# Optimization experiments

Hardware: AMD Instinct MI355X
Metric: run time of the kernel (lower is better)

Reference implementation:

```python
import jax, jax.numpy as jnp
import numpy as np

B = 32768      # batch
D = 512        # embedding dim
V = 100000     # vocab_length (row 0 reserved -> table has V+1 rows)
S = 100        # num_neg_samples (hard-coded in source)
DISTORTION = 0.4


def _expected_counts():
    # fixed_unigram sampler: zipf-ish counts, distorted by 0.4, 1 reserved id
    counts = 1.0 / np.arange(1, V + 1, dtype=np.float64)
    p = counts ** DISTORTION
    p = p / p.sum()
    q = np.zeros(V + 1, dtype=np.float64)
    # unique sampling expected count: E[id in sample] = 1-(1-p)^S
    q[1:] = -np.expm1(S * np.log1p(-p))
    q[0] = 1e-9  # reserved id, never sampled; avoid log(0)
    return q


def setup_inputs() -> dict:
    key = jax.random.key(0)
    k1, k2, k3, k4 = jax.random.split(key, 4)
    label = jax.random.randint(k1, (B,), 1, V + 1, dtype=jnp.int64)
    inputs = jax.random.normal(k2, (B, D), dtype=jnp.float32)
    weights = jax.random.normal(k3, (V + 1, D), dtype=jnp.float32) * 0.05
    biases = jnp.zeros((V + 1,), dtype=jnp.float32)
    sampled_ids = jax.random.choice(k4, V, (S,), replace=False).astype(jnp.int64) + 1
    q = jnp.asarray(_expected_counts(), dtype=jnp.float32)
    true_expected_count = q[label]          # [B]
    sampled_expected_count = q[sampled_ids]  # [S]
    return {
        "label": label, "inputs": inputs, "weights": weights, "biases": biases,
        "sampled_ids": sampled_ids,
        "true_expected_count": true_expected_count,
        "sampled_expected_count": sampled_expected_count,
    }


def reference(label, inputs, weights, biases, sampled_ids,
              true_expected_count, sampled_expected_count):
    # --- _compute_sampled_logits with subtract_log_q=True ---
    true_w = weights[label]                                   # [B, D] gather
    true_logits = (jnp.einsum('bd,bd->b', inputs, true_w)
                   + biases[label]
                   - jnp.log(true_expected_count))            # [B]
    samp_w = weights[sampled_ids]                             # [S, D] gather
    samp_logits = (jnp.einsum('bd,sd->bs', inputs, samp_w)
                   + biases[sampled_ids]
                   - jnp.log(sampled_expected_count))         # [B, S]
    logits = jnp.concatenate([true_logits[:, None], samp_logits], axis=1)  # [B, 1+S]
    # labels are one-hot at column 0 -> CE = logsumexp - true logit
    losses = jax.nn.logsumexp(logits, axis=1) - logits[:, 0]
    loss = jnp.mean(losses)
    return logits, loss
```

## Files before the change

kernel.cpp:

```cpp
#include <hip/hip_runtime.h>
#include <math.h>

#define B_TOT 32768
#define DIM   512
#define NS    100
#define NCOL  101
#define TB    128
#define NBLK  (B_TOT / TB)
#define WPITCH 520

typedef __attribute__((ext_vector_type(8))) short short8;
typedef __attribute__((ext_vector_type(4))) float f32x4;

static __device__ __forceinline__ short f2bf(float f) {
    unsigned u = __builtin_bit_cast(unsigned, f);
    unsigned r = (u + 0x7FFFu + ((u >> 16) & 1u)) >> 16;
    return (short)r;
}

__global__ __launch_bounds__(512)
void fused_kernel(const int* __restrict__ label,
                  const float* __restrict__ inputs,
                  const float* __restrict__ weights,
                  const float* __restrict__ biases,
                  const int* __restrict__ sids,
                  const float* __restrict__ tq,
                  const float* __restrict__ sq,
                  float* __restrict__ out,
                  float* __restrict__ lpart)
{
    __shared__ short W_lds[112 * WPITCH];
    __shared__ float base_lds[112];
    __shared__ int   s_sid[NS];
    __shared__ float ls_lds[8];

    const int t = threadIdx.x;

    if (t < NS) s_sid[t] = sids[t];
    __syncthreads();

    float4 sreg[25];
    #pragma unroll
    for (int q = 0; q < 25; q++) {
        const int idx = t + q * 512;
        sreg[q] = *(const float4*)(weights + (long)s_sid[idx >> 7] * DIM + (idx & 127) * 4);
    }
    #pragma unroll
    for (int q = 0; q < 25; q++) {
        const int idx = t + q * 512;
        *(short4*)&W_lds[(idx >> 7) * WPITCH + (idx & 127) * 4] =
            make_short4(f2bf(sreg[q].x), f2bf(sreg[q].y), f2bf(sreg[q].z), f2bf(sreg[q].w));
    }
    for (int idx = t; idx < 12 * (WPITCH / 4); idx += 512) {
        const int row = 100 + idx / (WPITCH / 4);
        const int kq  = (idx % (WPITCH / 4)) * 4;
        *(short4*)&W_lds[row * WPITCH + kq] = make_short4(0, 0, 0, 0);
    }
    if (t < 112)
        base_lds[t] = (t < NS) ? biases[s_sid[t]] - logf(sq[t]) : -INFINITY;

    const int wave = t >> 6;
    const int lane = t & 63;
    const int rit  = lane & 15;
    const int seg  = lane >> 4;
    const long b0  = (long)blockIdx.x * TB;
    const long absRow = b0 + wave * 16 + rit;
    const int lab = label[absRow];
    const float* aptr = inputs  + absRow * DIM + seg * 8;
    const float* wtp  = weights + (long)lab * DIM + seg * 8;

    f32x4 acc_r[7];
    #pragma unroll
    for (int c = 0; c < 7; c++) acc_r[c] = (f32x4){0.f, 0.f, 0.f, 0.f};

    float4 wr[8][2];
    float4 ar[8][2];
    #pragma unroll
    for (int p = 0; p < 8; p++) {
        wr[p][0] = *(const float4*)(wtp + p * 32);
        wr[p][1] = *(const float4*)(wtp + p * 32 + 4);
    }
    #pragma unroll
    for (int p = 0; p < 8; p++) {
        ar[p][0] = *(const float4*)(aptr + p * 32);
        ar[p][1] = *(const float4*)(aptr + p * 32 + 4);
    }

    asm volatile("s_waitcnt lgkmcnt(0)" ::: "memory");
    __builtin_amdgcn_s_barrier();

    float t0 = 0.f, t1 = 0.f;
    #pragma unroll
    for (int kc = 0; kc < 16; kc++) {
        const int sa = kc & 7, sw = kc & 7;
        const float4 a0 = ar[sa][0], a1 = ar[sa][1];
        const float4 w0 = wr[sw][0], w1 = wr[sw][1];
        if (kc + 8 < 16) {
            ar[sa][0] = *(const float4*)(aptr + (kc + 8) * 32);
            ar[sa][1] = *(const float4*)(aptr + (kc + 8) * 32 + 4);
            wr[sw][0] = *(const float4*)(wtp + (kc + 8) * 32);
            wr[sw][1] = *(const float4*)(wtp + (kc + 8) * 32 + 4);
        }

        t0 = fmaf(a0.x, w0.x, t0); t0 = fmaf(a0.y, w0.y, t0);
        t0 = fmaf(a0.z, w0.z, t0); t0 = fmaf(a0.w, w0.w, t0);
        t1 = fmaf(a1.x, w1.x, t1); t1 = fmaf(a1.y, w1.y, t1);
        t1 = fmaf(a1.z, w1.z, t1); t1 = fmaf(a1.w, w1.w, t1);

        short8 af;
        af[0] = f2bf(a0.x); af[1] = f2bf(a0.y); af[2] = f2bf(a0.z); af[3] = f2bf(a0.w);
        af[4] = f2bf(a1.x); af[5] = f2bf(a1.y); af[6] = f2bf(a1.z); af[7] = f2bf(a1.w);

        const int wko = kc * 32 + seg * 8;
        #pragma unroll
        for (int c = 0; c < 7; c++) {
            const short8 bf = *(const short8*)&W_lds[(c * 16 + rit) * WPITCH + wko];
            acc_r[c] = __builtin_amdgcn_mfma_f32_16x16x32_bf16(af, bf, acc_r[c], 0, 0, 0);
        }
    }
    float tacc = t0 + t1;

    tacc += __shfl_xor(tacc, 16);
    tacc += __shfl_xor(tacc, 32);
    const float tl = tacc + biases[lab] - logf(tq[absRow]);
    if (lane < 16) out[absRow * NCOL] = tl;

    const int g = lane >> 4;
    float base_v[7];
    #pragma unroll
    for (int c = 0; c < 7; c++) base_v[c] = base_lds[c * 16 + rit];

    float loss_sum = 0.f;
    #pragma unroll
    for (int i = 0; i < 4; i++) {
        const int r = g * 4 + i;
        const long orow = (b0 + wave * 16 + r) * NCOL;
        const float tlv = __shfl(tl, r);
        float v[7];
        float m = tlv;
        #pragma unroll
        for (int c = 0; c < 7; c++) {
            v[c] = acc_r[c][i] + base_v[c];
            m = fmaxf(m, v[c]);
        }
        #pragma unroll
        for (int off = 1; off < 16; off <<= 1) m = fmaxf(m, __shfl_xor(m, off));
        float s = (rit == 0) ? expf(tlv - m) : 0.f;
        #pragma unroll
        for (int c = 0; c < 7; c++) s += expf(v[c] - m);
        #pragma unroll
        for (int off = 1; off < 16; off <<= 1) s += __shfl_xor(s, off);
        loss_sum += m + logf(s) - tlv;
        #pragma unroll
        for (int c = 0; c < 7; c++) {
            const int col = c * 16 + rit;
            if (col < NS) out[orow + 1 + col] = v[c];
        }
    }
    float wl = (rit == 0) ? loss_sum : 0.f;
    wl += __shfl_xor(wl, 16);
    wl += __shfl_xor(wl, 32);
    if (lane == 0) ls_lds[wave] = wl;
    __syncthreads();
    if (t == 0) {
        float bp = 0.f;
        #pragma unroll
        for (int w = 0; w < 8; w++) bp += ls_lds[w];
        lpart[blockIdx.x] = bp;
    }
}

__global__ __launch_bounds__(64)
void reduce_kernel(const float* __restrict__ lpart, float* __restrict__ out_loss)
{
    const int lane = threadIdx.x;
    double s = 0.0;
    #pragma unroll
    for (int q = 0; q < 4; q++) s += (double)lpart[lane + q * 64];
    #pragma unroll
    for (int o = 32; o > 0; o >>= 1) {
        const double other = __shfl_down(s, o);
        s += other;
    }
    if (lane == 0) *out_loss = (float)(s * (1.0 / (double)B_TOT));
}

extern "C" void kernel_launch(void* const* d_in, const int* in_sizes, int n_in,
                              void* d_out, int out_size, void* d_ws, size_t ws_size,
                              hipStream_t stream)
{
    const int*   label   = (const int*)d_in[0];
    const float* inputs  = (const float*)d_in[1];
    const float* weights = (const float*)d_in[2];
    const float* biases  = (const float*)d_in[3];
    const int*   sids    = (const int*)d_in[4];
    const float* tq      = (const float*)d_in[5];
    const float* sq      = (const float*)d_in[6];
    float* out   = (float*)d_out;
    float* lpart = (float*)d_ws;

    fused_kernel<<<NBLK, 512, 0, stream>>>(label, inputs, weights, biases,
                                           sids, tq, sq, out, lpart);
    reduce_kernel<<<1, 64, 0, stream>>>(lpart, out + (long)B_TOT * NCOL);
}
```

Measured before the change: 35.61 us.

## Prepack sampled weights to bf16 in a separate kernel before fused pass

Adds a small pack kernel that gathers the 100 sampled weight rows, converts them to bf16 and zero-pads them to 112 rows in workspace, and precomputes the bias minus log-q vector. Each fused block now loads the packed bf16 tile with contiguous short8 loads, which halves the bytes per block and removes the indirect gather and per-block conversion. It also hoists the label bias and tq loads earlier. This costs an extra kernel launch and a dependency between kernels.

```diff
diff --git a/kernel.cpp b/kernel.cpp
--- a/kernel.cpp
+++ b/kernel.cpp
@@ -9,6 +9,9 @@
 #define NBLK  (B_TOT / TB)
 #define WPITCH 520
 
+#define BASE_BYTE  114688
+#define LPART_BYTE 115200
+
 typedef __attribute__((ext_vector_type(8))) short short8;
 typedef __attribute__((ext_vector_type(4))) float f32x4;
 
@@ -16,6 +19,25 @@
     unsigned u = __builtin_bit_cast(unsigned, f);
     unsigned r = (u + 0x7FFFu + ((u >> 16) & 1u)) >> 16;
     return (short)r;
+}
+
+__global__ __launch_bounds__(256)
+void pack_kernel(const float* __restrict__ weights, const float* __restrict__ biases,
+                 const int* __restrict__ sids, const float* __restrict__ sq,
+                 short* __restrict__ wpack, float* __restrict__ base_g)
+{
+    const int tid = blockIdx.x * 256 + threadIdx.x;
+    if (tid < 112)
+        base_g[tid] = (tid < NS) ? biases[sids[tid]] - logf(sq[tid]) : -INFINITY;
+    if (tid >= 112 * 128) return;
+    const int row = tid >> 7;
+    const int k4  = (tid & 127) * 4;
+    short4 v = make_short4(0, 0, 0, 0);
+    if (row < NS) {
+        const float4 f = *(const float4*)(weights + (long)sids[row] * DIM + k4);
+        v = make_short4(f2bf(f.x), f2bf(f.y), f2bf(f.z), f2bf(f.w));
+    }
+    *(short4*)&wpack[row * DIM + k4] = v;
 }
 
 __global__ __launch_bounds__(512)
@@ -23,49 +45,39 @@
                   const float* __restrict__ inputs,
                   const float* __restrict__ weights,
                   const float* __restrict__ biases,
-                  const int* __restrict__ sids,
                   const float* __restrict__ tq,
-                  const float* __restrict__ sq,
+                  const short* __restrict__ wpack,
+                  const float* __restrict__ base_g,
                   float* __restrict__ out,
                   float* __restrict__ lpart)
 {
     __shared__ short W_lds[112 * WPITCH];
-    __shared__ float base_lds[112];
-    __shared__ int   s_sid[NS];
     __shared__ float ls_lds[8];
 
-    const int t = threadIdx.x;
-
-    if (t < NS) s_sid[t] = sids[t];
-    __syncthreads();
-
-    float4 sreg[25];
-    #pragma unroll
-    for (int q = 0; q < 25; q++) {
-        const int idx = t + q * 512;
-        sreg[q] = *(const float4*)(weights + (long)s_sid[idx >> 7] * DIM + (idx & 127) * 4);
-    }
-    #pragma unroll
-    for (int q = 0; q < 25; q++) {
-        const int idx = t + q * 512;
-        *(short4*)&W_lds[(idx >> 7) * WPITCH + (idx & 127) * 4] =
-            make_short4(f2bf(sreg[q].x), f2bf(sreg[q].y), f2bf(sreg[q].z), f2bf(sreg[q].w));
-    }
-    for (int idx = t; idx < 12 * (WPITCH / 4); idx += 512) {
-        const int row = 100 + idx / (WPITCH / 4);
-        const int kq  = (idx % (WPITCH / 4)) * 4;
-        *(short4*)&W_lds[row * WPITCH + kq] = make_short4(0, 0, 0, 0);
-    }
-    if (t < 112)
-        base_lds[t] = (t < NS) ? biases[s_sid[t]] - logf(sq[t]) : -INFINITY;
-
+    const int t    = threadIdx.x;
     const int wave = t >> 6;
     const int lane = t & 63;
     const int rit  = lane & 15;
     const int seg  = lane >> 4;
     const long b0  = (long)blockIdx.x * TB;
     const long absRow = b0 + wave * 16 + rit;
+
     const int lab = label[absRow];
+    const float tqv = tq[absRow];
+
+    short8 sreg[14];
+    #pragma unroll
+    for (int q = 0; q < 14; q++)
+        sreg[q] = *(const short8*)(wpack + (t + q * 512) * 8);
+    float base_v[7];
+    #pragma unroll
+    for (int c = 0; c < 7; c++) base_v[c] = base_g[c * 16 + rit];
+    #pragma unroll
+    for (int q = 0; q < 14; q++) {
+        const int idx = t + q * 512;
+        *(short8*)&W_lds[(idx >> 6) * WPITCH + (idx & 63) * 8] = sreg[q];
+    }
+
     const float* aptr = inputs  + absRow * DIM + seg * 8;
     const float* wtp  = weights + (long)lab * DIM + seg * 8;
 
@@ -85,6 +97,7 @@
         ar[p][0] = *(const float4*)(aptr + p * 32);
         ar[p][1] = *(const float4*)(aptr + p * 32 + 4);
     }
+    const float bias_lab = biases[lab];
 
     asm volatile("s_waitcnt lgkmcnt(0)" ::: "memory");
     __builtin_amdgcn_s_barrier();
@@ -92,14 +105,14 @@
     float t0 = 0.f, t1 = 0.f;
     #pragma unroll
     for (int kc = 0; kc < 16; kc++) {
-        const int sa = kc & 7, sw = kc & 7;
+        const int sa = kc & 7;
         const float4 a0 = ar[sa][0], a1 = ar[sa][1];
-        const float4 w0 = wr[sw][0], w1 = wr[sw][1];
+        const float4 w0 = wr[sa][0], w1 = wr[sa][1];
         if (kc + 8 < 16) {
             ar[sa][0] = *(const float4*)(aptr + (kc + 8) * 32);
             ar[sa][1] = *(const float4*)(aptr + (kc + 8) * 32 + 4);
-            wr[sw][0] = *(const float4*)(wtp + (kc + 8) * 32);
-            wr[sw][1] = *(const float4*)(wtp + (kc + 8) * 32 + 4);
+            wr[sa][0] = *(const float4*)(wtp + (kc + 8) * 32);
+            wr[sa][1] = *(const float4*)(wtp + (kc + 8) * 32 + 4);
         }
 
         t0 = fmaf(a0.x, w0.x, t0); t0 = fmaf(a0.y, w0.y, t0);
@@ -122,14 +135,10 @@
 
     tacc += __shfl_xor(tacc, 16);
     tacc += __shfl_xor(tacc, 32);
-    const float tl = tacc + biases[lab] - logf(tq[absRow]);
+    const float tl = tacc + bias_lab - logf(tqv);
     if (lane < 16) out[absRow * NCOL] = tl;
 
     const int g = lane >> 4;
-    float base_v[7];
-    #pragma unroll
-    for (int c = 0; c < 7; c++) base_v[c] = base_lds[c * 16 + rit];
-
     float loss_sum = 0.f;
     #pragma unroll
     for (int i = 0; i < 4; i++) {
@@ -196,10 +205,13 @@
     const int*   sids    = (const int*)d_in[4];
     const float* tq      = (const float*)d_in[5];
     const float* sq      = (const float*)d_in[6];
-    float* out   = (float*)d_out;
-    float* lpart = (float*)d_ws;
-
-    fused_kernel<<<NBLK, 512, 0, stream>>>(label, inputs, weights, biases,
-                                           sids, tq, sq, out, lpart);
+    float* out    = (float*)d_out;
+    short* wpack  = (short*)d_ws;
+    float* base_g = (float*)((char*)d_ws + BASE_BYTE);
+    float* lpart  = (float*)((char*)d_ws + LPART_BYTE);
+
+    pack_kernel<<<56, 256, 0, stream>>>(weights, biases, sids, sq, wpack, base_g);
+    fused_kernel<<<NBLK, 512, 0, stream>>>(label, inputs, weights, biases, tq,
+                                           wpack, base_g, out, lpart);
     reduce_kernel<<<1, 64, 0, stream>>>(lpart, out + (long)B_TOT * NCOL);
 }
```

Measured after the change: 37.82 us. 6.2% more time.
